# Kernel optimization log

Hardware: AMD Instinct MI355X
Metric: run time of the kernel (lower is better)

The kernel has to match this reference:

```python
import jax, jax.numpy as jnp
import numpy as np

DT_SCALER = 1.0 / 24.0
EULER_STEPS = 10   # odeint euler, t in [0,1], step_size=0.1
STEP = 0.1


def setup_inputs() -> dict:
    key = jax.random.key(0)
    ks = jax.random.split(key, 10)
    B, T, D, H = 8192, 100, 16, 32
    Hd = min((H + D) * 2, 50)  # 50
    x = jax.random.normal(ks[0], (B, T, D), dtype=jnp.float32)
    dt = jax.random.uniform(ks[1], (B, T, 2), dtype=jnp.float32)
    # dh MLP: Linear(H+D -> Hd), tanh, Linear(Hd -> H), tanh ; init N(0, 0.1), bias 0
    W1 = 0.1 * jax.random.normal(ks[2], (Hd, H + D), dtype=jnp.float32)
    b1 = jnp.zeros((Hd,), jnp.float32)
    W2 = 0.1 * jax.random.normal(ks[3], (H, Hd), dtype=jnp.float32)
    b2 = jnp.zeros((H,), jnp.float32)
    # dy MLP: Linear(H -> 2H), tanh, Linear(2H -> 1)
    W3 = 0.1 * jax.random.normal(ks[4], (2 * H, H), dtype=jnp.float32)
    b3 = jnp.zeros((2 * H,), jnp.float32)
    W4 = 0.1 * jax.random.normal(ks[5], (1, 2 * H), dtype=jnp.float32)
    b4 = jnp.zeros((1,), jnp.float32)
    return {"dt": dt, "x": x, "W1": W1, "b1": b1, "W2": W2, "b2": b2,
            "W3": W3, "b3": b3, "W4": W4, "b4": b4}


def _forward(dt, x, W1, b1, W2, b2, W3, b3, W4, b4):
    B, T, D = x.shape
    H = W2.shape[0]
    dti = (dt[:, :, 1] - dt[:, :, 0])[..., None]  # [B,T,1]
    x_t = jnp.swapaxes(x, 0, 1)      # [T,B,D]
    dt_t = jnp.swapaxes(dti, 0, 1)   # [T,B,1]

    def time_step(h, inp):
        x_i, dt_i = inp              # [B,D], [B,1]
        y = x_i[:, 0:1]              # z0 y-part reset to observation each step
        scale = dt_i * DT_SCALER     # [B,1]

        def euler(carry, _):
            y, h = carry
            dh = jnp.tanh(jnp.tanh(jnp.concatenate([x_i, h], axis=1) @ W1.T + b1) @ W2.T + b2) * scale
            dy = (jnp.tanh(h @ W3.T + b3) @ W4.T + b4) * scale
            return (y + STEP * dy, h + STEP * dh), None

        (y, h), _ = jax.lax.scan(euler, (y, h), None, length=EULER_STEPS)
        return h, y

    h0 = jnp.zeros((B, H), jnp.float32)
    _, mu = jax.lax.scan(time_step, h0, (x_t, dt_t))  # mu: [T,B,1]
    return jnp.swapaxes(mu, 0, 1)                     # [B,T,1]


def reference(dt, x, W1, b1, W2, b2, W3, b3, W4, b4):
    return _forward(dt, x, W1, b1, W2, b2, W3, b3, W4, b4)
```

## Files before the change

kernel.cpp:

```cpp
#include <hip/hip_runtime.h>
#include <stdint.h>

#define T_STEPS 100
#define D_IN 16
#define H_DIM 32
#define HD 50
#define KXH 48
#define EULER 10
#define STEPF 0.1f
#define DT_SCALERF (1.0f/24.0f)
#define TANH_SCALE 2.8853900817779268f

typedef __attribute__((ext_vector_type(8))) short short8;
typedef __attribute__((ext_vector_type(4))) float float4v;
typedef __attribute__((ext_vector_type(2))) uint32_t uint2v;
typedef __attribute__((ext_vector_type(4))) uint32_t uint4v;

__device__ __forceinline__ float tanh_pre(float us) {
    float e = __builtin_amdgcn_exp2f(us);
    return 1.0f - 2.0f * __builtin_amdgcn_rcpf(e + 1.0f);
}
__device__ __forceinline__ uint32_t f2bf_u(float f) {
    uint32_t u = __builtin_bit_cast(uint32_t, f);
    return u + 0x7fffu + ((u >> 16) & 1u);
}
__device__ __forceinline__ uint32_t pack2(float lo, float hi) {
    return (f2bf_u(hi) & 0xffff0000u) | (f2bf_u(lo) >> 16);
}
__device__ __forceinline__ short f2bf(float f) { return (short)(f2bf_u(f) >> 16); }

__global__ __launch_bounds__(512, 4) void latode_kernel(
    const float* __restrict__ dt, const float* __restrict__ x,
    const float* __restrict__ W1, const float* __restrict__ b1,
    const float* __restrict__ W2, const float* __restrict__ b2,
    const float* __restrict__ W3, const float* __restrict__ b3,
    const float* __restrict__ W4, const float* __restrict__ b4,
    float* __restrict__ out)
{
    const int tid  = threadIdx.x;
    const int wave = tid >> 6;
    const int lane = tid & 63;
    const int n16  = lane & 15;
    const int quad = lane >> 4;
    const int b0   = blockIdx.x * 16;
    const int mt   = wave & 3;
    const bool is_u1 = (wave < 4);

    __shared__ __align__(16) uint32_t hbuf[16 * 20];
    __shared__ __align__(16) uint32_t zbuf[16 * 36];
    __shared__ float pbuf[64];

    for (int i = tid; i < 16 * 20; i += 512) hbuf[i] = 0;
    for (int i = tid; i < 16 * 36; i += 512) zbuf[i] = 0;

    short8 wA[2];
    float4v bA, w4v;
    if (is_u1) {
        int m = mt * 16 + n16;
#pragma unroll
        for (int kt = 0; kt < 2; ++kt)
#pragma unroll
            for (int j = 0; j < 8; ++j) {
                int kk = kt * 32 + quad * 8 + j;
                float w = 0.0f;
                if (m < HD) {
                    if (kk < 32)      w = W1[m * KXH + 16 + kk];
                    else if (kk < 48) w = W1[m * KXH + (kk - 32)];
                }
                wA[kt][j] = f2bf(w * TANH_SCALE);
            }
#pragma unroll
        for (int r = 0; r < 4; ++r) {
            int f = mt * 16 + quad * 4 + r;
            bA[r] = (f < HD) ? b1[f] * TANH_SCALE : 0.0f;
        }
    } else {
        int m = mt * 16 + n16;
#pragma unroll
        for (int j = 0; j < 8; ++j)
            wA[0][j] = f2bf(W3[m * H_DIM + quad * 8 + j] * TANH_SCALE);
#pragma unroll
        for (int r = 0; r < 4; ++r) {
            int f = mt * 16 + quad * 4 + r;
            bA[r] = b3[f] * TANH_SCALE;
            w4v[r] = W4[f];
        }
    }
    short8 w2f[2];
    float4v b2v;
    if (wave >= 6) {
        int m = (wave - 6) * 16 + n16;
#pragma unroll
        for (int kt = 0; kt < 2; ++kt)
#pragma unroll
            for (int j = 0; j < 8; ++j) {
                int kk = kt * 32 + quad * 8 + j;
                w2f[kt][j] = f2bf(kk < HD ? W2[m * HD + kk] * TANH_SCALE : 0.0f);
            }
#pragma unroll
        for (int r = 0; r < 4; ++r)
            b2v[r] = b2[(wave - 6) * 16 + quad * 4 + r] * TANH_SCALE;
    }
    const float b4s = b4[0];

    float4v hC = (float4v){0.f, 0.f, 0.f, 0.f};

    const float* xrow = x + (size_t)(b0 + n16) * (T_STEPS * D_IN);
    const float* drow = dt + (size_t)(b0 + n16) * (T_STEPS * 2);
    float4 xa = {0,0,0,0}, xb = {0,0,0,0};
    float2 dtv = {0.f, 0.f};
    float y0 = 0.f;
    if (is_u1 && quad < 2) {
        xa = *(const float4*)(xrow + quad * 8);
        xb = *(const float4*)(xrow + quad * 8 + 4);
    }
    if (wave == 4 || wave >= 6) dtv = *(const float2*)(drow);
    if (wave == 4) y0 = xrow[0];

    __syncthreads();

#pragma unroll 1
    for (int t = 0; t < T_STEPS; ++t) {
        short8 xB = (short8){0,0,0,0,0,0,0,0};
        if (is_u1 && quad < 2) {
            uint4v xp;
            xp[0] = pack2(xa.x, xa.y); xp[1] = pack2(xa.z, xa.w);
            xp[2] = pack2(xb.x, xb.y); xp[3] = pack2(xb.z, xb.w);
            xB = __builtin_bit_cast(short8, xp);
        }
        const float scl = (dtv.y - dtv.x) * DT_SCALERF;
        const float s10 = STEPF * scl;
        const float y0c = y0;
        float psum = 0.f;

        {
            int tn = (t + 1 < T_STEPS) ? t + 1 : (T_STEPS - 1);
            if (is_u1 && quad < 2) {
                xa = *(const float4*)(xrow + tn * D_IN + quad * 8);
                xb = *(const float4*)(xrow + tn * D_IN + quad * 8 + 4);
            }
            if (wave == 4 || wave >= 6) dtv = *(const float2*)(drow + tn * 2);
            if (wave == 4) y0 = xrow[tn * D_IN];
        }

#pragma unroll 1
        for (int e = 0; e < EULER; ++e) {
            short8 hB = __builtin_bit_cast(short8, *(const uint4v*)&hbuf[n16 * 20 + quad * 4]);

            if (is_u1) {
                float4v a = bA;
                a = __builtin_amdgcn_mfma_f32_16x16x32_bf16(wA[0], hB, a, 0, 0, 0);
                a = __builtin_amdgcn_mfma_f32_16x16x32_bf16(wA[1], xB, a, 0, 0, 0);
                if (wave < 3) {
                    float z0 = tanh_pre(a[0]), z1 = tanh_pre(a[1]);
                    float z2 = tanh_pre(a[2]), z3 = tanh_pre(a[3]);
                    *(uint2v*)&zbuf[n16 * 36 + mt * 8 + quad * 2] =
                        (uint2v){pack2(z0, z1), pack2(z2, z3)};
                } else {
                    float z0 = tanh_pre(a[0]), z1 = tanh_pre(a[1]);
                    if (quad == 0) zbuf[n16 * 36 + 24] = pack2(z0, z1);
                }
            } else {
                float4v a = bA;
                a = __builtin_amdgcn_mfma_f32_16x16x32_bf16(wA[0], hB, a, 0, 0, 0);
                float pacc = w4v[0] * tanh_pre(a[0]) + w4v[1] * tanh_pre(a[1])
                           + w4v[2] * tanh_pre(a[2]) + w4v[3] * tanh_pre(a[3]);
                pacc += __shfl_xor(pacc, 16, 64);
                pacc += __shfl_xor(pacc, 32, 64);
                if (lane < 16) pbuf[mt * 16 + n16] = pacc;
            }
            __syncthreads();

            if (wave >= 6) {
                short8 zB0 = __builtin_bit_cast(short8, *(const uint4v*)&zbuf[n16 * 36 + quad * 4]);
                short8 zB1 = __builtin_bit_cast(short8, *(const uint4v*)&zbuf[n16 * 36 + 16 + quad * 4]);
                float4v u2 = b2v;
                u2 = __builtin_amdgcn_mfma_f32_16x16x32_bf16(w2f[0], zB0, u2, 0, 0, 0);
                u2 = __builtin_amdgcn_mfma_f32_16x16x32_bf16(w2f[1], zB1, u2, 0, 0, 0);
                hC[0] += s10 * tanh_pre(u2[0]);
                hC[1] += s10 * tanh_pre(u2[1]);
                hC[2] += s10 * tanh_pre(u2[2]);
                hC[3] += s10 * tanh_pre(u2[3]);
                *(uint2v*)&hbuf[n16 * 20 + (wave - 6) * 8 + quad * 2] =
                    (uint2v){pack2(hC[0], hC[1]), pack2(hC[2], hC[3])};
            } else if (wave == 4) {
                psum += pbuf[n16] + pbuf[16 + n16] + pbuf[32 + n16] + pbuf[48 + n16];
            }
            __syncthreads();
        }

        if (wave == 4 && quad == 0) {
            float y = y0c + STEPF * scl * (psum + (float)EULER * b4s);
            out[(size_t)(b0 + n16) * T_STEPS + t] = y;
        }
    }
}

extern "C" void kernel_launch(void* const* d_in, const int* in_sizes, int n_in,
                              void* d_out, int out_size, void* d_ws, size_t ws_size,
                              hipStream_t stream) {
    const float* dt = (const float*)d_in[0];
    const float* x  = (const float*)d_in[1];
    const float* W1 = (const float*)d_in[2];
    const float* b1 = (const float*)d_in[3];
    const float* W2 = (const float*)d_in[4];
    const float* b2 = (const float*)d_in[5];
    const float* W3 = (const float*)d_in[6];
    const float* b3 = (const float*)d_in[7];
    const float* W4 = (const float*)d_in[8];
    const float* b4 = (const float*)d_in[9];
    float* out = (float*)d_out;

    const int B = 8192;
    dim3 grid(B / 16), block(512);
    latode_kernel<<<grid, block, 0, stream>>>(dt, x, W1, b1, W2, b2, W3, b3, W4, b4, out);
}
```

Before: 762.4 us.

## Fuse both dh MLP layers into one wave with register-resident hidden state

The block shrinks from 8 waves to 2. One wave computes both layers of the dh MLP entirely in registers, permuting the W1 and W2 rows so the first MFMA's tanh output can be repacked straight into the second MFMA's B operand without going through LDS. The other wave evaluates the dy MLP from a double-buffered LDS copy of h, so each Euler step needs one barrier instead of two. The x projection is hoisted out of the Euler loop, the biases are folded into the matmuls through constant-one input entries, and bf16 packing now uses the hardware v_cvt_pk_bf16_f32 instruction. The trade-off is far fewer waves per CU and a longer serial dependency chain inside a single wave.

```diff
diff --git a/kernel.cpp b/kernel.cpp
--- a/kernel.cpp
+++ b/kernel.cpp
@@ -13,23 +13,32 @@
 
 typedef __attribute__((ext_vector_type(8))) short short8;
 typedef __attribute__((ext_vector_type(4))) float float4v;
-typedef __attribute__((ext_vector_type(2))) uint32_t uint2v;
 typedef __attribute__((ext_vector_type(4))) uint32_t uint4v;
 
 __device__ __forceinline__ float tanh_pre(float us) {
     float e = __builtin_amdgcn_exp2f(us);
     return 1.0f - 2.0f * __builtin_amdgcn_rcpf(e + 1.0f);
 }
-__device__ __forceinline__ uint32_t f2bf_u(float f) {
+__device__ __forceinline__ uint32_t pkbf(float lo, float hi) {
+    uint32_t r;
+    asm("v_cvt_pk_bf16_f32 %0, %1, %2" : "=v"(r) : "v"(lo), "v"(hi));
+    return r;
+}
+__device__ __forceinline__ short f2bf(float f) {
     uint32_t u = __builtin_bit_cast(uint32_t, f);
-    return u + 0x7fffu + ((u >> 16) & 1u);
-}
-__device__ __forceinline__ uint32_t pack2(float lo, float hi) {
-    return (f2bf_u(hi) & 0xffff0000u) | (f2bf_u(lo) >> 16);
-}
-__device__ __forceinline__ short f2bf(float f) { return (short)(f2bf_u(f) >> 16); }
-
-__global__ __launch_bounds__(512, 4) void latode_kernel(
+    u = u + 0x7fffu + ((u >> 16) & 1u);
+    return (short)(u >> 16);
+}
+
+__device__ __forceinline__ int zorig(int kk) {
+    int f = kk >> 5, q = (kk >> 3) & 3, jj = kk & 7;
+    int t = 2 * f + (jj >> 2), r = jj & 3;
+    if (t < 3) return t * 16 + q * 4 + r;
+    if (r == 0 && q < 2) return 48 + q;
+    return -1;
+}
+
+__global__ __launch_bounds__(128, 1) void latode_kernel(
     const float* __restrict__ dt, const float* __restrict__ x,
     const float* __restrict__ W1, const float* __restrict__ b1,
     const float* __restrict__ W2, const float* __restrict__ b2,
@@ -43,155 +52,179 @@
     const int n16  = lane & 15;
     const int quad = lane >> 4;
     const int b0   = blockIdx.x * 16;
-    const int mt   = wave & 3;
-    const bool is_u1 = (wave < 4);
-
-    __shared__ __align__(16) uint32_t hbuf[16 * 20];
-    __shared__ __align__(16) uint32_t zbuf[16 * 36];
-    __shared__ float pbuf[64];
-
-    for (int i = tid; i < 16 * 20; i += 512) hbuf[i] = 0;
-    for (int i = tid; i < 16 * 36; i += 512) zbuf[i] = 0;
-
-    short8 wA[2];
-    float4v bA, w4v;
-    if (is_u1) {
-        int m = mt * 16 + n16;
-#pragma unroll
-        for (int kt = 0; kt < 2; ++kt)
+
+    __shared__ __align__(16) uint32_t hslot[2][256];
+
+    for (int i = tid; i < 512; i += 128) ((uint32_t*)hslot)[i] = 0;
+
+    const float* xrow = x + (size_t)(b0 + n16) * (T_STEPS * D_IN);
+    const float* drow = dt + (size_t)(b0 + n16) * (T_STEPS * 2);
+
+    short8 w1h[4], w1x[4], w2f[2][2];
+    short8 w3f[4];
+    float4v b3v[4], w4v4[4];
+
+    if (wave == 0) {
+#pragma unroll
+        for (int t = 0; t < 4; ++t) {
+            int kz = 32 * (t >> 1) + 8 * (n16 >> 2) + 4 * (t & 1) + (n16 & 3);
+            int of = zorig(kz);
+#pragma unroll
+            for (int j = 0; j < 8; ++j) {
+                int kk = quad * 8 + j;
+                float wh = 0.0f, wx = 0.0f;
+                if (of >= 0) {
+                    wh = W1[of * KXH + 16 + kk];
+                    if (kk < 16)       wx = W1[of * KXH + kk];
+                    else if (kk == 16) wx = b1[of];
+                }
+                w1h[t][j] = f2bf(wh * TANH_SCALE);
+                w1x[t][j] = f2bf(wx * TANH_SCALE);
+            }
+        }
+#pragma unroll
+        for (int t2 = 0; t2 < 2; ++t2) {
+            int hrow = 8 * (n16 >> 2) + 4 * t2 + (n16 & 3);
+#pragma unroll
+            for (int kt = 0; kt < 2; ++kt)
 #pragma unroll
             for (int j = 0; j < 8; ++j) {
                 int kk = kt * 32 + quad * 8 + j;
+                int oz = zorig(kk);
                 float w = 0.0f;
-                if (m < HD) {
-                    if (kk < 32)      w = W1[m * KXH + 16 + kk];
-                    else if (kk < 48) w = W1[m * KXH + (kk - 32)];
-                }
-                wA[kt][j] = f2bf(w * TANH_SCALE);
-            }
-#pragma unroll
-        for (int r = 0; r < 4; ++r) {
-            int f = mt * 16 + quad * 4 + r;
-            bA[r] = (f < HD) ? b1[f] * TANH_SCALE : 0.0f;
+                if (oz >= 0)       w = W2[hrow * HD + oz];
+                else if (kk == 63) w = b2[hrow];
+                w2f[t2][kt][j] = f2bf(w * TANH_SCALE);
+            }
         }
     } else {
-        int m = mt * 16 + n16;
-#pragma unroll
-        for (int j = 0; j < 8; ++j)
-            wA[0][j] = f2bf(W3[m * H_DIM + quad * 8 + j] * TANH_SCALE);
-#pragma unroll
-        for (int r = 0; r < 4; ++r) {
-            int f = mt * 16 + quad * 4 + r;
-            bA[r] = b3[f] * TANH_SCALE;
-            w4v[r] = W4[f];
-        }
-    }
-    short8 w2f[2];
-    float4v b2v;
-    if (wave >= 6) {
-        int m = (wave - 6) * 16 + n16;
-#pragma unroll
-        for (int kt = 0; kt < 2; ++kt)
-#pragma unroll
-            for (int j = 0; j < 8; ++j) {
-                int kk = kt * 32 + quad * 8 + j;
-                w2f[kt][j] = f2bf(kk < HD ? W2[m * HD + kk] * TANH_SCALE : 0.0f);
-            }
-#pragma unroll
-        for (int r = 0; r < 4; ++r)
-            b2v[r] = b2[(wave - 6) * 16 + quad * 4 + r] * TANH_SCALE;
+#pragma unroll
+        for (int t = 0; t < 4; ++t) {
+            int f = t * 16 + n16;
+#pragma unroll
+            for (int j = 0; j < 8; ++j)
+                w3f[t][j] = f2bf(W3[f * H_DIM + quad * 8 + j] * TANH_SCALE);
+#pragma unroll
+            for (int r = 0; r < 4; ++r) {
+                int fr = t * 16 + quad * 4 + r;
+                b3v[t][r]  = b3[fr] * TANH_SCALE;
+                w4v4[t][r] = W4[fr];
+            }
+        }
     }
     const float b4s = b4[0];
 
-    float4v hC = (float4v){0.f, 0.f, 0.f, 0.f};
-
-    const float* xrow = x + (size_t)(b0 + n16) * (T_STEPS * D_IN);
-    const float* drow = dt + (size_t)(b0 + n16) * (T_STEPS * 2);
+    float4v hC0 = {0.f,0.f,0.f,0.f}, hC1 = {0.f,0.f,0.f,0.f};
+    short8  hB  = {0,0,0,0,0,0,0,0};
+    const uint32_t z1d3 = (quad == 3) ? 0x3f800000u : 0u;
+    const float4v zero4 = {0.f,0.f,0.f,0.f};
+
     float4 xa = {0,0,0,0}, xb = {0,0,0,0};
-    float2 dtv = {0.f, 0.f};
+    float2 dtv = {0.f,0.f};
     float y0 = 0.f;
-    if (is_u1 && quad < 2) {
-        xa = *(const float4*)(xrow + quad * 8);
-        xb = *(const float4*)(xrow + quad * 8 + 4);
+    if (wave == 0) {
+        if (quad < 2) { xa = *(const float4*)(xrow + quad * 8);
+                        xb = *(const float4*)(xrow + quad * 8 + 4); }
+        dtv = *(const float2*)drow;
+    } else {
+        dtv = *(const float2*)drow;
+        y0  = xrow[0];
     }
-    if (wave == 4 || wave >= 6) dtv = *(const float2*)(drow);
-    if (wave == 4) y0 = xrow[0];
 
     __syncthreads();
 
 #pragma unroll 1
     for (int t = 0; t < T_STEPS; ++t) {
-        short8 xB = (short8){0,0,0,0,0,0,0,0};
-        if (is_u1 && quad < 2) {
-            uint4v xp;
-            xp[0] = pack2(xa.x, xa.y); xp[1] = pack2(xa.z, xa.w);
-            xp[2] = pack2(xb.x, xb.y); xp[3] = pack2(xb.z, xb.w);
-            xB = __builtin_bit_cast(short8, xp);
-        }
-        const float scl = (dtv.y - dtv.x) * DT_SCALERF;
-        const float s10 = STEPF * scl;
+        const float s10 = (dtv.y - dtv.x) * (DT_SCALERF * STEPF);
         const float y0c = y0;
         float psum = 0.f;
 
+        float4v cxa[4];
+        if (wave == 0) {
+            uint4v xp = {0,0,0,0};
+            if (quad < 2) {
+                xp[0] = pkbf(xa.x, xa.y); xp[1] = pkbf(xa.z, xa.w);
+                xp[2] = pkbf(xb.x, xb.y); xp[3] = pkbf(xb.z, xb.w);
+            } else if (quad == 2) {
+                xp[0] = 0x00003f80u;
+            }
+            short8 xB = __builtin_bit_cast(short8, xp);
+#pragma unroll
+            for (int tt = 0; tt < 4; ++tt)
+                cxa[tt] = __builtin_amdgcn_mfma_f32_16x16x32_bf16(w1x[tt], xB, zero4, 0, 0, 0);
+        }
+
         {
             int tn = (t + 1 < T_STEPS) ? t + 1 : (T_STEPS - 1);
-            if (is_u1 && quad < 2) {
-                xa = *(const float4*)(xrow + tn * D_IN + quad * 8);
-                xb = *(const float4*)(xrow + tn * D_IN + quad * 8 + 4);
-            }
-            if (wave == 4 || wave >= 6) dtv = *(const float2*)(drow + tn * 2);
-            if (wave == 4) y0 = xrow[tn * D_IN];
-        }
-
-#pragma unroll 1
+            if (wave == 0) {
+                if (quad < 2) { xa = *(const float4*)(xrow + tn * D_IN + quad * 8);
+                                xb = *(const float4*)(xrow + tn * D_IN + quad * 8 + 4); }
+                dtv = *(const float2*)(drow + tn * 2);
+            } else {
+                dtv = *(const float2*)(drow + tn * 2);
+                y0  = xrow[tn * D_IN];
+            }
+        }
+
+#pragma unroll 2
         for (int e = 0; e < EULER; ++e) {
-            short8 hB = __builtin_bit_cast(short8, *(const uint4v*)&hbuf[n16 * 20 + quad * 4]);
-
-            if (is_u1) {
-                float4v a = bA;
-                a = __builtin_amdgcn_mfma_f32_16x16x32_bf16(wA[0], hB, a, 0, 0, 0);
-                a = __builtin_amdgcn_mfma_f32_16x16x32_bf16(wA[1], xB, a, 0, 0, 0);
-                if (wave < 3) {
-                    float z0 = tanh_pre(a[0]), z1 = tanh_pre(a[1]);
-                    float z2 = tanh_pre(a[2]), z3 = tanh_pre(a[3]);
-                    *(uint2v*)&zbuf[n16 * 36 + mt * 8 + quad * 2] =
-                        (uint2v){pack2(z0, z1), pack2(z2, z3)};
-                } else {
-                    float z0 = tanh_pre(a[0]), z1 = tanh_pre(a[1]);
-                    if (quad == 0) zbuf[n16 * 36 + 24] = pack2(z0, z1);
-                }
+            if (wave == 0) {
+                float4v a0 = __builtin_amdgcn_mfma_f32_16x16x32_bf16(w1h[0], hB, cxa[0], 0, 0, 0);
+                float4v a1 = __builtin_amdgcn_mfma_f32_16x16x32_bf16(w1h[1], hB, cxa[1], 0, 0, 0);
+                float4v a2 = __builtin_amdgcn_mfma_f32_16x16x32_bf16(w1h[2], hB, cxa[2], 0, 0, 0);
+                float4v a3 = __builtin_amdgcn_mfma_f32_16x16x32_bf16(w1h[3], hB, cxa[3], 0, 0, 0);
+                uint4v z0, z1;
+                z0[0] = pkbf(tanh_pre(a0[0]), tanh_pre(a0[1]));
+                z0[1] = pkbf(tanh_pre(a0[2]), tanh_pre(a0[3]));
+                z0[2] = pkbf(tanh_pre(a1[0]), tanh_pre(a1[1]));
+                z0[3] = pkbf(tanh_pre(a1[2]), tanh_pre(a1[3]));
+                z1[0] = pkbf(tanh_pre(a2[0]), tanh_pre(a2[1]));
+                z1[1] = pkbf(tanh_pre(a2[2]), tanh_pre(a2[3]));
+                z1[2] = pkbf(tanh_pre(a3[0]), 0.0f);
+                z1[3] = z1d3;
+                short8 zf0 = __builtin_bit_cast(short8, z0);
+                short8 zf1 = __builtin_bit_cast(short8, z1);
+                float4v u20 = __builtin_amdgcn_mfma_f32_16x16x32_bf16(w2f[0][0], zf0, zero4, 0, 0, 0);
+                u20 = __builtin_amdgcn_mfma_f32_16x16x32_bf16(w2f[0][1], zf1, u20, 0, 0, 0);
+                float4v u21 = __builtin_amdgcn_mfma_f32_16x16x32_bf16(w2f[1][0], zf0, zero4, 0, 0, 0);
+                u21 = __builtin_amdgcn_mfma_f32_16x16x32_bf16(w2f[1][1], zf1, u21, 0, 0, 0);
+                hC0[0] += s10 * tanh_pre(u20[0]);
+                hC0[1] += s10 * tanh_pre(u20[1]);
+                hC0[2] += s10 * tanh_pre(u20[2]);
+                hC0[3] += s10 * tanh_pre(u20[3]);
+                hC1[0] += s10 * tanh_pre(u21[0]);
+                hC1[1] += s10 * tanh_pre(u21[1]);
+                hC1[2] += s10 * tanh_pre(u21[2]);
+                hC1[3] += s10 * tanh_pre(u21[3]);
+                uint4v hp;
+                hp[0] = pkbf(hC0[0], hC0[1]); hp[1] = pkbf(hC0[2], hC0[3]);
+                hp[2] = pkbf(hC1[0], hC1[1]); hp[3] = pkbf(hC1[2], hC1[3]);
+                hB = __builtin_bit_cast(short8, hp);
+                *(uint4v*)&hslot[(e + 1) & 1][lane * 4] = hp;
             } else {
-                float4v a = bA;
-                a = __builtin_amdgcn_mfma_f32_16x16x32_bf16(wA[0], hB, a, 0, 0, 0);
-                float pacc = w4v[0] * tanh_pre(a[0]) + w4v[1] * tanh_pre(a[1])
-                           + w4v[2] * tanh_pre(a[2]) + w4v[3] * tanh_pre(a[3]);
+                short8 hb = __builtin_bit_cast(short8, *(const uint4v*)&hslot[e & 1][lane * 4]);
+                float4v a0 = __builtin_amdgcn_mfma_f32_16x16x32_bf16(w3f[0], hb, b3v[0], 0, 0, 0);
+                float4v a1 = __builtin_amdgcn_mfma_f32_16x16x32_bf16(w3f[1], hb, b3v[1], 0, 0, 0);
+                float4v a2 = __builtin_amdgcn_mfma_f32_16x16x32_bf16(w3f[2], hb, b3v[2], 0, 0, 0);
+                float4v a3 = __builtin_amdgcn_mfma_f32_16x16x32_bf16(w3f[3], hb, b3v[3], 0, 0, 0);
+                float p0 = w4v4[0][0]*tanh_pre(a0[0]) + w4v4[0][1]*tanh_pre(a0[1])
+                         + w4v4[0][2]*tanh_pre(a0[2]) + w4v4[0][3]*tanh_pre(a0[3]);
+                float p1 = w4v4[1][0]*tanh_pre(a1[0]) + w4v4[1][1]*tanh_pre(a1[1])
+                         + w4v4[1][2]*tanh_pre(a1[2]) + w4v4[1][3]*tanh_pre(a1[3]);
+                float p2 = w4v4[2][0]*tanh_pre(a2[0]) + w4v4[2][1]*tanh_pre(a2[1])
+                         + w4v4[2][2]*tanh_pre(a2[2]) + w4v4[2][3]*tanh_pre(a2[3]);
+                float p3 = w4v4[3][0]*tanh_pre(a3[0]) + w4v4[3][1]*tanh_pre(a3[1])
+                         + w4v4[3][2]*tanh_pre(a3[2]) + w4v4[3][3]*tanh_pre(a3[3]);
+                float pacc = (p0 + p1) + (p2 + p3);
                 pacc += __shfl_xor(pacc, 16, 64);
                 pacc += __shfl_xor(pacc, 32, 64);
-                if (lane < 16) pbuf[mt * 16 + n16] = pacc;
+                psum += pacc;
             }
             __syncthreads();
-
-            if (wave >= 6) {
-                short8 zB0 = __builtin_bit_cast(short8, *(const uint4v*)&zbuf[n16 * 36 + quad * 4]);
-                short8 zB1 = __builtin_bit_cast(short8, *(const uint4v*)&zbuf[n16 * 36 + 16 + quad * 4]);
-                float4v u2 = b2v;
-                u2 = __builtin_amdgcn_mfma_f32_16x16x32_bf16(w2f[0], zB0, u2, 0, 0, 0);
-                u2 = __builtin_amdgcn_mfma_f32_16x16x32_bf16(w2f[1], zB1, u2, 0, 0, 0);
-                hC[0] += s10 * tanh_pre(u2[0]);
-                hC[1] += s10 * tanh_pre(u2[1]);
-                hC[2] += s10 * tanh_pre(u2[2]);
-                hC[3] += s10 * tanh_pre(u2[3]);
-                *(uint2v*)&hbuf[n16 * 20 + (wave - 6) * 8 + quad * 2] =
-                    (uint2v){pack2(hC[0], hC[1]), pack2(hC[2], hC[3])};
-            } else if (wave == 4) {
-                psum += pbuf[n16] + pbuf[16 + n16] + pbuf[32 + n16] + pbuf[48 + n16];
-            }
-            __syncthreads();
-        }
-
-        if (wave == 4 && quad == 0) {
-            float y = y0c + STEPF * scl * (psum + (float)EULER * b4s);
-            out[(size_t)(b0 + n16) * T_STEPS + t] = y;
+        }
+
+        if (wave == 1 && lane < 16) {
+            out[(size_t)(b0 + n16) * T_STEPS + t] = y0c + s10 * (psum + (float)EULER * b4s);
         }
     }
 }
@@ -212,6 +245,6 @@
     float* out = (float*)d_out;
 
     const int B = 8192;
-    dim3 grid(B / 16), block(512);
+    dim3 grid(B / 16), block(128);
     latode_kernel<<<grid, block, 0, stream>>>(dt, x, W1, b1, W2, b2, W3, b3, W4, b4, out);
 }
```

New measurement: 803.1 us. +5.3%, slower.
